# Optimization experiments

Measured on AMD Instinct MI355X. Metric: run time of the kernel, lower is better.

## Reference

```python
import jax, jax.numpy as jnp
import numpy as np

EMBED_DIM = 768
NUM_HEADS = 12
HEAD_DIM = EMBED_DIM // NUM_HEADS


def setup_inputs() -> dict:
    key = jax.random.key(0)
    ks = jax.random.split(key, 9)
    B, S, E = 8, 1024, EMBED_DIM
    scale = 1.0 / np.sqrt(E)
    inputs = jax.random.normal(ks[0], (B, S, E), dtype=jnp.float32)
    Wq = jax.random.normal(ks[1], (E, E), dtype=jnp.float32) * scale
    Wk = jax.random.normal(ks[2], (E, E), dtype=jnp.float32) * scale
    Wv = jax.random.normal(ks[3], (E, E), dtype=jnp.float32) * scale
    Wo = jax.random.normal(ks[4], (E, E), dtype=jnp.float32) * scale
    bq = jnp.zeros((E,), dtype=jnp.float32)
    bk = jnp.zeros((E,), dtype=jnp.float32)
    bv = jnp.zeros((E,), dtype=jnp.float32)
    bo = jnp.zeros((E,), dtype=jnp.float32)
    return {"inputs": inputs, "Wq": Wq, "bq": bq, "Wk": Wk, "bk": bk,
            "Wv": Wv, "bv": bv, "Wo": Wo, "bo": bo}


def reference(inputs, Wq, bq, Wk, bk, Wv, bv, Wo, bo):
    B, S, E = inputs.shape
    H, D = NUM_HEADS, HEAD_DIM

    def split_heads(x):  # [B,S,E] -> [B,H,S,D]
        return x.reshape(B, S, H, D).transpose(0, 2, 1, 3)

    q = split_heads(inputs @ Wq + bq)
    k = split_heads(inputs @ Wk + bk)
    v = split_heads(inputs @ Wv + bv)

    # scaled dot-product attention; note: scale uses sqrt(last dim of key) = sqrt(D)
    score = jnp.einsum('bhqd,bhkd->bhqk', q, k) / jnp.sqrt(jnp.float32(D))
    weights = jax.nn.softmax(score, axis=-1)
    attn = jnp.einsum('bhqk,bhkd->bhqd', weights, v)  # [B,H,S,D]

    concat = attn.transpose(0, 2, 1, 3).reshape(B, S, E)
    return concat @ Wo + bo
```

## Files before the change

kernel.cpp:

```cpp
#include <hip/hip_runtime.h>
#include <hip/hip_bf16.h>
#include <cstddef>

#define E_DIM  768
#define S_LEN  1024
#define NHEADS 12
#define HDIM   64
#define BATCH  8
#define TOKENS (BATCH * S_LEN)
#define WELEMS (E_DIM * E_DIM)

typedef short bf16x8 __attribute__((ext_vector_type(8)));
typedef short bf16x4 __attribute__((ext_vector_type(4)));
typedef float f32x4  __attribute__((ext_vector_type(4)));

#define MFMA16(a, b, c) __builtin_amdgcn_mfma_f32_16x16x32_bf16((a), (b), (c), 0, 0, 0)

#define GLD_LDS16(gp, lp)                                                  \
    __builtin_amdgcn_global_load_lds(                                      \
        (const __attribute__((address_space(1))) void*)(gp),               \
        (__attribute__((address_space(3))) void*)(lp), 16, 0, 0)

static __device__ __forceinline__ short f2bf(float f) {
    union { float f; unsigned int u; } cv; cv.f = f;
    unsigned int u = cv.u + 0x7fffu + ((cv.u >> 16) & 1u);
    return (short)(u >> 16);
}

__global__ __launch_bounds__(256) void xcvt_kernel(
    const float* __restrict__ X, short* __restrict__ Y)
{
    const size_t i = ((size_t)blockIdx.x * 256 + threadIdx.x) * 8;
    const float4 a = *(const float4*)&X[i];
    const float4 b = *(const float4*)&X[i + 4];
    bf16x8 o;
    o[0] = f2bf(a.x); o[1] = f2bf(a.y); o[2] = f2bf(a.z); o[3] = f2bf(a.w);
    o[4] = f2bf(b.x); o[5] = f2bf(b.y); o[6] = f2bf(b.z); o[7] = f2bf(b.w);
    *(bf16x8*)&Y[i] = o;
}

__global__ __launch_bounds__(256) void transpose_w(
    const float* __restrict__ s0, const float* __restrict__ s1,
    const float* __restrict__ s2, const float* __restrict__ s3,
    short* __restrict__ dst)
{
    const int z = blockIdx.z;
    const float* S = (z == 0) ? s0 : (z == 1) ? s1 : (z == 2) ? s2 : s3;
    short* D = dst + (size_t)z * WELEMS;
    __shared__ float t[64][65];
    const int r = threadIdx.x >> 2, c0 = (threadIdx.x & 3) * 16;
    const int br = blockIdx.x * 64, bc = blockIdx.y * 64;
    #pragma unroll
    for (int j = 0; j < 4; ++j) {
        float4 v = *(const float4*)&S[(size_t)(br + r) * E_DIM + bc + c0 + j * 4];
        t[r][c0 + j * 4 + 0] = v.x; t[r][c0 + j * 4 + 1] = v.y;
        t[r][c0 + j * 4 + 2] = v.z; t[r][c0 + j * 4 + 3] = v.w;
    }
    __syncthreads();
    #pragma unroll
    for (int half = 0; half < 2; ++half) {
        bf16x8 o;
        #pragma unroll
        for (int j = 0; j < 8; ++j) o[j] = f2bf(t[c0 + half * 8 + j][r]);
        *(bf16x8*)&D[(size_t)(bc + r) * E_DIM + br + c0 + half * 8] = o;
    }
}

template<bool AF32>
__global__ __launch_bounds__(256, 3) void gemm_qkv_t(
    const void* __restrict__ Ap, const short* __restrict__ Wt,
    const float* __restrict__ bq, const float* __restrict__ bk,
    const float* __restrict__ bv, short* __restrict__ oq,
    short* __restrict__ ok, short* __restrict__ ov)
{
    __shared__ __align__(16) short As[128 * 64];
    __shared__ __align__(16) short Bs[128 * 64];

    const int tid  = threadIdx.x;
    const int wave = tid >> 6, lane = tid & 63;
    const int quad = lane >> 4, l16 = lane & 15;
    const int bm = blockIdx.x * 128;
    const int by = blockIdx.y;
    const int wsel = by / 6;
    const int nb = (by % 6) * 128;
    const short* wt = Wt + (size_t)wsel * WELEMS;
    const float* bias = (wsel == 0) ? bq : (wsel == 1) ? bk : bv;
    short* outp = (wsel == 0) ? oq : (wsel == 1) ? ok : ov;
    const int wm = (wave >> 1) * 64, wn = (wave & 1) * 64;

    f32x4 acc[4][4];
    #pragma unroll
    for (int mt = 0; mt < 4; ++mt)
        #pragma unroll
        for (int nt = 0; nt < 4; ++nt) acc[mt][nt] = (f32x4){0.f, 0.f, 0.f, 0.f};

    for (int k0 = 0; k0 < E_DIM; k0 += 64) {
        if (AF32) {
            const float* A = (const float*)Ap;
            float4 ax[4][2];
            #pragma unroll
            for (int i = 0; i < 4; ++i) {
                const int slot = i * 256 + tid;
                const int row = slot >> 3, cl = slot & 7;
                const float4* gp = (const float4*)&A[(size_t)(bm + row) * E_DIM + k0 + cl * 8];
                ax[i][0] = gp[0]; ax[i][1] = gp[1];
            }
            __syncthreads();
            #pragma unroll
            for (int i = 0; i < 4; ++i) {
                const int slot = i * 256 + tid;
                const int row = slot >> 3, cl = slot & 7, cg = cl ^ (row & 7);
                GLD_LDS16(&wt[(size_t)(nb + row) * E_DIM + k0 + cg * 8], &Bs[slot * 8]);
            }
            #pragma unroll
            for (int i = 0; i < 4; ++i) {
                const int slot = i * 256 + tid;
                const int row = slot >> 3, cl = slot & 7, cs = cl ^ (row & 7);
                bf16x8 v8;
                v8[0] = f2bf(ax[i][0].x); v8[1] = f2bf(ax[i][0].y);
                v8[2] = f2bf(ax[i][0].z); v8[3] = f2bf(ax[i][0].w);
                v8[4] = f2bf(ax[i][1].x); v8[5] = f2bf(ax[i][1].y);
                v8[6] = f2bf(ax[i][1].z); v8[7] = f2bf(ax[i][1].w);
                *(bf16x8*)&As[row * 64 + cs * 8] = v8;
            }
        } else {
            const short* A = (const short*)Ap;
            __syncthreads();
            #pragma unroll
            for (int i = 0; i < 4; ++i) {
                const int slot = i * 256 + tid;
                const int row = slot >> 3, cl = slot & 7, cg = cl ^ (row & 7);
                GLD_LDS16(&A[(size_t)(bm + row) * E_DIM + k0 + cg * 8], &As[slot * 8]);
            }
            #pragma unroll
            for (int i = 0; i < 4; ++i) {
                const int slot = i * 256 + tid;
                const int row = slot >> 3, cl = slot & 7, cg = cl ^ (row & 7);
                GLD_LDS16(&wt[(size_t)(nb + row) * E_DIM + k0 + cg * 8], &Bs[slot * 8]);
            }
        }
        __syncthreads();

        #pragma unroll
        for (int ks = 0; ks < 2; ++ks) {
            bf16x8 a[4], b[4];
            #pragma unroll
            for (int mt = 0; mt < 4; ++mt) {
                const int row = wm + mt * 16 + l16;
                const int c = (ks * 4 + quad) ^ (row & 7);
                a[mt] = *(const bf16x8*)&As[row * 64 + c * 8];
            }
            #pragma unroll
            for (int nt = 0; nt < 4; ++nt) {
                const int row = wn + nt * 16 + l16;
                const int c = (ks * 4 + quad) ^ (row & 7);
                b[nt] = *(const bf16x8*)&Bs[row * 64 + c * 8];
            }
            #pragma unroll
            for (int mt = 0; mt < 4; ++mt)
                #pragma unroll
                for (int nt = 0; nt < 4; ++nt)
                    acc[mt][nt] = MFMA16(a[mt], b[nt], acc[mt][nt]);
        }
    }

    const float qscale = (wsel == 0) ? 0.125f : 1.0f;
    #pragma unroll
    for (int nt = 0; nt < 4; ++nt) {
        const int ncol = nb + wn + nt * 16 + l16;
        const float bvv = bias[ncol];
        const int h = ncol >> 6, d = ncol & (HDIM - 1);
        #pragma unroll
        for (int mt = 0; mt < 4; ++mt) {
            const int grow = bm + wm + mt * 16 + quad * 4;
            if (wsel < 2) {
                #pragma unroll
                for (int r = 0; r < 4; ++r) {
                    const int g = grow + r, b = g >> 10, s = g & (S_LEN - 1);
                    outp[((size_t)(b * NHEADS + h) * S_LEN + s) * HDIM + d] =
                        f2bf((acc[mt][nt][r] + bvv) * qscale);
                }
            } else {
                const int b = grow >> 10, s0 = grow & (S_LEN - 1);
                bf16x4 pv;
                #pragma unroll
                for (int r = 0; r < 4; ++r) pv[r] = f2bf(acc[mt][nt][r] + bvv);
                *(bf16x4*)&outp[((size_t)(b * NHEADS + h) * HDIM + d) * S_LEN + s0] = pv;
            }
        }
    }
}

__global__ __launch_bounds__(256, 3) void gemm_out_kernel(
    const short* __restrict__ A, const short* __restrict__ Wt,
    const float* __restrict__ bias, float* __restrict__ out)
{
    __shared__ __align__(16) short As[128 * 64];
    __shared__ __align__(16) short Bs[128 * 64];

    const int tid  = threadIdx.x;
    const int wave = tid >> 6, lane = tid & 63;
    const int quad = lane >> 4, l16 = lane & 15;
    const int bm = blockIdx.x * 128, nb = blockIdx.y * 128;
    const int wm = (wave >> 1) * 64, wn = (wave & 1) * 64;

    f32x4 acc[4][4];
    #pragma unroll
    for (int mt = 0; mt < 4; ++mt)
        #pragma unroll
        for (int nt = 0; nt < 4; ++nt) acc[mt][nt] = (f32x4){0.f, 0.f, 0.f, 0.f};

    for (int k0 = 0; k0 < E_DIM; k0 += 64) {
        __syncthreads();
        #pragma unroll
        for (int i = 0; i < 4; ++i) {
            const int slot = i * 256 + tid;
            const int row = slot >> 3, cl = slot & 7, cg = cl ^ (row & 7);
            GLD_LDS16(&A[(size_t)(bm + row) * E_DIM + k0 + cg * 8], &As[slot * 8]);
        }
        #pragma unroll
        for (int i = 0; i < 4; ++i) {
            const int slot = i * 256 + tid;
            const int row = slot >> 3, cl = slot & 7, cg = cl ^ (row & 7);
            GLD_LDS16(&Wt[(size_t)(nb + row) * E_DIM + k0 + cg * 8], &Bs[slot * 8]);
        }
        __syncthreads();

        #pragma unroll
        for (int ks = 0; ks < 2; ++ks) {
            bf16x8 a[4], b[4];
            #pragma unroll
            for (int mt = 0; mt < 4; ++mt) {
                const int row = wm + mt * 16 + l16;
                const int c = (ks * 4 + quad) ^ (row & 7);
                a[mt] = *(const bf16x8*)&As[row * 64 + c * 8];
            }
            #pragma unroll
            for (int nt = 0; nt < 4; ++nt) {
                const int row = wn + nt * 16 + l16;
                const int c = (ks * 4 + quad) ^ (row & 7);
                b[nt] = *(const bf16x8*)&Bs[row * 64 + c * 8];
            }
            #pragma unroll
            for (int mt = 0; mt < 4; ++mt)
                #pragma unroll
                for (int nt = 0; nt < 4; ++nt)
                    acc[mt][nt] = MFMA16(a[mt], b[nt], acc[mt][nt]);
        }
    }

    #pragma unroll
    for (int nt = 0; nt < 4; ++nt) {
        const int ncol = nb + wn + nt * 16 + l16;
        const float bvv = bias[ncol];
        #pragma unroll
        for (int mt = 0; mt < 4; ++mt) {
            const int grow = bm + wm + mt * 16 + quad * 4;
            #pragma unroll
            for (int r = 0; r < 4; ++r)
                out[(size_t)(grow + r) * E_DIM + ncol] = acc[mt][nt][r] + bvv;
        }
    }
}

__global__ __launch_bounds__(256) void attn_kernel(
    const short* __restrict__ Q, const short* __restrict__ K,
    const short* __restrict__ V, short* __restrict__ O)
{
    __shared__ __align__(16) short Ps[128 * 72];
    __shared__ __align__(16) short Ks[64 * 64];
    __shared__ __align__(16) short Vt[64 * 64];

    const int tid  = threadIdx.x;
    const int wave = tid >> 6, lane = tid & 63;
    const int quad = lane >> 4, l16 = lane & 15;
    const int q0 = blockIdx.x * 128;
    const int bh = blockIdx.y;
    const size_t base = (size_t)bh * S_LEN * HDIM;
    const short* Qb = Q + base;
    const short* Kb = K + base;
    const short* Vb = V + base;

    bf16x8 qa[2][2];
    #pragma unroll
    for (int mt = 0; mt < 2; ++mt)
        #pragma unroll
        for (int ks = 0; ks < 2; ++ks)
            qa[mt][ks] = *(const bf16x8*)&Qb[
                (size_t)(q0 + wave * 32 + mt * 16 + l16) * HDIM + ks * 32 + quad * 8];

    bf16x8 ones;
    #pragma unroll
    for (int j = 0; j < 8; ++j) ones[j] = (short)0x3F80;

    f32x4 oacc[2][4], lacc[2];
    #pragma unroll
    for (int mt = 0; mt < 2; ++mt) {
        #pragma unroll
        for (int nt = 0; nt < 4; ++nt) oacc[mt][nt] = (f32x4){0.f, 0.f, 0.f, 0.f};
        lacc[mt] = (f32x4){0.f, 0.f, 0.f, 0.f};
    }

    for (int kt = 0; kt < S_LEN; kt += 64) {
        __syncthreads();
        #pragma unroll
        for (int i = 0; i < 2; ++i) {
            const int slot = i * 256 + tid;
            const int row = slot >> 3, cl = slot & 7, cg = cl ^ (row & 7);
            GLD_LDS16(&Kb[(size_t)(kt + row) * HDIM + cg * 8], &Ks[slot * 8]);
        }
        #pragma unroll
        for (int i = 0; i < 2; ++i) {
            const int slot = i * 256 + tid;
            const int row = slot >> 3, cl = slot & 7, cg = cl ^ (row & 7);
            GLD_LDS16(&Vb[(size_t)row * S_LEN + kt + cg * 8], &Vt[slot * 8]);
        }
        __syncthreads();

        f32x4 sc[2][4];
        #pragma unroll
        for (int mt = 0; mt < 2; ++mt)
            #pragma unroll
            for (int nt = 0; nt < 4; ++nt) sc[mt][nt] = (f32x4){0.f, 0.f, 0.f, 0.f};
        #pragma unroll
        for (int ks = 0; ks < 2; ++ks)
            #pragma unroll
            for (int nt = 0; nt < 4; ++nt) {
                const int row = nt * 16 + l16;
                const int c = (ks * 4 + quad) ^ (row & 7);
                const bf16x8 kf = *(const bf16x8*)&Ks[row * 64 + c * 8];
                #pragma unroll
                for (int mt = 0; mt < 2; ++mt)
                    sc[mt][nt] = MFMA16(qa[mt][ks], kf, sc[mt][nt]);
            }

        #pragma unroll
        for (int mt = 0; mt < 2; ++mt) {
            const int prow = wave * 32 + mt * 16 + quad * 4;
            #pragma unroll
            for (int nt = 0; nt < 4; ++nt)
                #pragma unroll
                for (int r = 0; r < 4; ++r)
                    Ps[(prow + r) * 72 + nt * 16 + l16] = f2bf(__expf(sc[mt][nt][r]));
        }

        bf16x8 pa[2][2];
        #pragma unroll
        for (int mt = 0; mt < 2; ++mt)
            #pragma unroll
            for (int ks = 0; ks < 2; ++ks)
                pa[mt][ks] = *(const bf16x8*)&Ps[(wave * 32 + mt * 16 + l16) * 72 + ks * 32 + quad * 8];

        #pragma unroll
        for (int ks = 0; ks < 2; ++ks) {
            #pragma unroll
            for (int nt = 0; nt < 4; ++nt) {
                const int row = nt * 16 + l16;
                const int c = (ks * 4 + quad) ^ (row & 7);
                const bf16x8 vf = *(const bf16x8*)&Vt[row * 64 + c * 8];
                #pragma unroll
                for (int mt = 0; mt < 2; ++mt)
                    oacc[mt][nt] = MFMA16(pa[mt][ks], vf, oacc[mt][nt]);
            }
            #pragma unroll
            for (int mt = 0; mt < 2; ++mt)
                lacc[mt] = MFMA16(pa[mt][ks], ones, lacc[mt]);
        }
    }

    const int b = bh / NHEADS, h = bh - b * NHEADS;
    #pragma unroll
    for (int mt = 0; mt < 2; ++mt)
        #pragma unroll
        for (int nt = 0; nt < 4; ++nt)
            #pragma unroll
            for (int r = 0; r < 4; ++r) {
                const int qrow = q0 + wave * 32 + mt * 16 + quad * 4 + r;
                const float val = oacc[mt][nt][r] / lacc[mt][r];
                O[(size_t)(b * S_LEN + qrow) * E_DIM + h * HDIM + nt * 16 + l16] = f2bf(val);
            }
}

extern "C" void kernel_launch(void* const* d_in, const int* in_sizes, int n_in,
                              void* d_out, int out_size, void* d_ws, size_t ws_size,
                              hipStream_t stream) {
    const float* X  = (const float*)d_in[0];
    const float* Wq = (const float*)d_in[1];
    const float* bq = (const float*)d_in[2];
    const float* Wk = (const float*)d_in[3];
    const float* bk = (const float*)d_in[4];
    const float* Wv = (const float*)d_in[5];
    const float* bv = (const float*)d_in[6];
    const float* Wo = (const float*)d_in[7];
    const float* bo = (const float*)d_in[8];
    float* out = (float*)d_out;

    const size_t t = (size_t)TOKENS * E_DIM;
    short* q    = (short*)d_ws;
    short* k    = q + t;
    short* vT   = k + t;
    short* attn = vT + t;

    const size_t fast_need = (5 * t + 4 * (size_t)WELEMS) * 2;
    if (ws_size >= fast_need) {
        short* wt4 = attn + t;
        short* xbf = wt4 + 4 * (size_t)WELEMS;
        xcvt_kernel<<<(TOKENS * E_DIM / 8) / 256, 256, 0, stream>>>(X, xbf);
        transpose_w<<<dim3(12, 12, 4), 256, 0, stream>>>(Wq, Wk, Wv, Wo, wt4);
        gemm_qkv_t<false><<<dim3(TOKENS / 128, 18), 256, 0, stream>>>(
            xbf, wt4, bq, bk, bv, q, k, vT);
        attn_kernel<<<dim3(S_LEN / 128, BATCH * NHEADS), 256, 0, stream>>>(q, k, vT, attn);
        gemm_out_kernel<<<dim3(TOKENS / 128, 6), 256, 0, stream>>>(
            attn, wt4 + 3 * (size_t)WELEMS, bo, out);
    } else {
        short* wt_qkv = attn;
        short* wt_o   = q;
        transpose_w<<<dim3(12, 12, 3), 256, 0, stream>>>(Wq, Wk, Wv, Wv, wt_qkv);
        gemm_qkv_t<true><<<dim3(TOKENS / 128, 18), 256, 0, stream>>>(
            X, wt_qkv, bq, bk, bv, q, k, vT);
        attn_kernel<<<dim3(S_LEN / 128, BATCH * NHEADS), 256, 0, stream>>>(q, k, vT, attn);
        transpose_w<<<dim3(12, 12, 1), 256, 0, stream>>>(Wo, Wo, Wo, Wo, wt_o);
        gemm_out_kernel<<<dim3(TOKENS / 128, 6), 256, 0, stream>>>(attn, wt_o, bo, out);
    }
}
```

Before: 200.3 us.

## Keep softmax probabilities in registers by transposing QK^T and using K16 MFMA

```diff
diff --git a/kernel.cpp b/kernel.cpp
--- a/kernel.cpp
+++ b/kernel.cpp
@@ -14,7 +14,8 @@
 typedef short bf16x4 __attribute__((ext_vector_type(4)));
 typedef float f32x4  __attribute__((ext_vector_type(4)));
 
-#define MFMA16(a, b, c) __builtin_amdgcn_mfma_f32_16x16x32_bf16((a), (b), (c), 0, 0, 0)
+#define MFMA16(a, b, c)   __builtin_amdgcn_mfma_f32_16x16x32_bf16((a), (b), (c), 0, 0, 0)
+#define MFMA16K16(a, b, c) __builtin_amdgcn_mfma_f32_16x16x16bf16_1k((a), (b), (c), 0, 0, 0)
 
 #define GLD_LDS16(gp, lp)                                                  \
     __builtin_amdgcn_global_load_lds(                                      \
@@ -267,7 +268,6 @@
     const short* __restrict__ Q, const short* __restrict__ K,
     const short* __restrict__ V, short* __restrict__ O)
 {
-    __shared__ __align__(16) short Ps[128 * 72];
     __shared__ __align__(16) short Ks[64 * 64];
     __shared__ __align__(16) short Vt[64 * 64];
 
@@ -289,9 +289,9 @@
             qa[mt][ks] = *(const bf16x8*)&Qb[
                 (size_t)(q0 + wave * 32 + mt * 16 + l16) * HDIM + ks * 32 + quad * 8];
 
-    bf16x8 ones;
-    #pragma unroll
-    for (int j = 0; j < 8; ++j) ones[j] = (short)0x3F80;
+    bf16x4 ones4;
+    #pragma unroll
+    for (int j = 0; j < 4; ++j) ones4[j] = (short)0x3F80;
 
     f32x4 oacc[2][4], lacc[2];
     #pragma unroll
@@ -321,50 +321,42 @@
         #pragma unroll
         for (int mt = 0; mt < 2; ++mt)
             #pragma unroll
-            for (int nt = 0; nt < 4; ++nt) sc[mt][nt] = (f32x4){0.f, 0.f, 0.f, 0.f};
+            for (int t = 0; t < 4; ++t) sc[mt][t] = (f32x4){0.f, 0.f, 0.f, 0.f};
         #pragma unroll
         for (int ks = 0; ks < 2; ++ks)
+            #pragma unroll
+            for (int t = 0; t < 4; ++t) {
+                const int row = t * 16 + l16;
+                const int c = (ks * 4 + quad) ^ (row & 7);
+                const bf16x8 kf = *(const bf16x8*)&Ks[row * 64 + c * 8];
+                #pragma unroll
+                for (int mt = 0; mt < 2; ++mt)
+                    sc[mt][t] = MFMA16(kf, qa[mt][ks], sc[mt][t]);
+            }
+
+        bf16x4 pa16[2][4];
+        #pragma unroll
+        for (int mt = 0; mt < 2; ++mt)
+            #pragma unroll
+            for (int t = 0; t < 4; ++t)
+                #pragma unroll
+                for (int r = 0; r < 4; ++r)
+                    pa16[mt][t][r] = f2bf(__expf(sc[mt][t][r]));
+
+        #pragma unroll
+        for (int t = 0; t < 4; ++t) {
+            #pragma unroll
+            for (int mt = 0; mt < 2; ++mt)
+                lacc[mt] = MFMA16K16(pa16[mt][t], ones4, lacc[mt]);
             #pragma unroll
             for (int nt = 0; nt < 4; ++nt) {
                 const int row = nt * 16 + l16;
-                const int c = (ks * 4 + quad) ^ (row & 7);
-                const bf16x8 kf = *(const bf16x8*)&Ks[row * 64 + c * 8];
+                const int c = (t * 2 + (quad >> 1)) ^ (row & 7);
+                const bf16x4 vb = *(const bf16x4*)&Vt[row * 64 + c * 8 + (quad & 1) * 4];
                 #pragma unroll
                 for (int mt = 0; mt < 2; ++mt)
-                    sc[mt][nt] = MFMA16(qa[mt][ks], kf, sc[mt][nt]);
-            }
-
-        #pragma unroll
-        for (int mt = 0; mt < 2; ++mt) {
-            const int prow = wave * 32 + mt * 16 + quad * 4;
-            #pragma unroll
-            for (int nt = 0; nt < 4; ++nt)
-                #pragma unroll
-                for (int r = 0; r < 4; ++r)
-                    Ps[(prow + r) * 72 + nt * 16 + l16] = f2bf(__expf(sc[mt][nt][r]));
-        }
-
-        bf16x8 pa[2][2];
-        #pragma unroll
-        for (int mt = 0; mt < 2; ++mt)
-            #pragma unroll
-            for (int ks = 0; ks < 2; ++ks)
-                pa[mt][ks] = *(const bf16x8*)&Ps[(wave * 32 + mt * 16 + l16) * 72 + ks * 32 + quad * 8];
-
-        #pragma unroll
-        for (int ks = 0; ks < 2; ++ks) {
-            #pragma unroll
-            for (int nt = 0; nt < 4; ++nt) {
-                const int row = nt * 16 + l16;
-                const int c = (ks * 4 + quad) ^ (row & 7);
-                const bf16x8 vf = *(const bf16x8*)&Vt[row * 64 + c * 8];
-                #pragma unroll
-                for (int mt = 0; mt < 2; ++mt)
-                    oacc[mt][nt] = MFMA16(pa[mt][ks], vf, oacc[mt][nt]);
-            }
-            #pragma unroll
-            for (int mt = 0; mt < 2; ++mt)
-                lacc[mt] = MFMA16(pa[mt][ks], ones, lacc[mt]);
+                    oacc[mt][nt] = MFMA16K16(pa16[mt][t], vb, oacc[mt][nt]);
+            }
         }
     }
 
```

After: 199.4 us. No clear change (-0.5%).
